# Optimization experiments

Measured on AMD Instinct MI355X. Metric: run time of the kernel, lower is better.

The kernel has to match this reference:

```python
import jax, jax.numpy as jnp
import numpy as np

NEG_SLOPE = 0.2  # PyG GATConv default negative_slope
EPS = 1e-16      # PyG softmax denominator eps


def gat_layer(x, src, dst, W, a_src, a_dst, num_nodes):
    """One GATConv (eval mode, self-loops already appended to src/dst).
    x: [N, Fin], W: [Fin, H*C], a_src/a_dst: [H, C]. Returns [N, H, C]."""
    H, C = a_src.shape
    h = (x @ W).reshape(num_nodes, H, C)                  # [N,H,C]
    alpha_src = jnp.sum(h * a_src, axis=-1)               # [N,H]
    alpha_dst = jnp.sum(h * a_dst, axis=-1)               # [N,H]
    e = alpha_src[src] + alpha_dst[dst]                   # [E,H]
    e = jnp.where(e > 0, e, NEG_SLOPE * e)                # leaky_relu
    # segment softmax keyed by destination node
    m = jax.ops.segment_max(e, dst, num_segments=num_nodes)   # [N,H]
    ex = jnp.exp(e - m[dst])                              # [E,H]
    s = jax.ops.segment_sum(ex, dst, num_segments=num_nodes)  # [N,H]
    alpha = ex / (s[dst] + EPS)                           # [E,H]
    # weighted scatter-aggregation of source features
    msg = h[src] * alpha[..., None]                       # [E,H,C]
    out = jax.ops.segment_sum(msg, dst, num_segments=num_nodes)  # [N,H,C]
    return out


def setup_inputs() -> dict:
    key = jax.random.key(0)
    ks = jax.random.split(key, 10)
    N, E = 50000, 800000
    Fin, C1, H, Fout = 128, 32, 8, 1
    x = jax.random.normal(ks[0], (N, Fin), dtype=jnp.float32)
    edge_index = jax.random.randint(ks[1], (2, E), 0, N).astype(jnp.int64)
    sc = 0.1
    W1 = jax.random.normal(ks[2], (Fin, H * C1), dtype=jnp.float32) * sc
    att_src1 = jax.random.normal(ks[3], (H, C1), dtype=jnp.float32) * sc
    att_dst1 = jax.random.normal(ks[4], (H, C1), dtype=jnp.float32) * sc
    bias1 = jnp.zeros((H * C1,), dtype=jnp.float32)
    W2 = jax.random.normal(ks[5], (H * C1, Fout), dtype=jnp.float32) * sc
    att_src2 = jax.random.normal(ks[6], (1, Fout), dtype=jnp.float32) * sc
    att_dst2 = jax.random.normal(ks[7], (1, Fout), dtype=jnp.float32) * sc
    bias2 = jnp.zeros((Fout,), dtype=jnp.float32)
    return {"x": x, "edge_index": edge_index, "W1": W1, "att_src1": att_src1,
            "att_dst1": att_dst1, "bias1": bias1, "W2": W2, "att_src2": att_src2,
            "att_dst2": att_dst2, "bias2": bias2}


def reference(x, edge_index, W1, att_src1, att_dst1, bias1, W2, att_src2, att_dst2, bias2):
    N = x.shape[0]
    loops = jnp.arange(N, dtype=edge_index.dtype)
    src = jnp.concatenate([edge_index[0], loops])   # add_self_loops=True
    dst = jnp.concatenate([edge_index[1], loops])
    # layer 1: heads=8, concat=True
    h1 = gat_layer(x, src, dst, W1, att_src1, att_dst1, N)      # [N,H,C1]
    h1 = h1.reshape(N, -1) + bias1                               # [N,H*C1]
    h1 = jax.nn.elu(h1)
    # layer 2: heads=1, concat=False (single head -> identity mean)
    h2 = gat_layer(h1, src, dst, W2, att_src2, att_dst2, N)      # [N,1,1]
    h2 = h2.reshape(N, -1) + bias2                               # [N,1]
    return jax.nn.sigmoid(h2).squeeze(-1)                        # [N]
```

## Files before the change

### kernel.cpp

```cpp
#include <hip/hip_runtime.h>
#include <math.h>

#define NEG_SLOPE 0.2f
#define GAT_EPS 1e-16f
#define NEG_BIG -3.0e38f
#define LOG2E 1.4426950408889634f
#define MAXDEG 96
#define BCAP 6144
#define CHUNK 2048
#define PREPB 136

typedef __attribute__((ext_vector_type(8))) short short8;
typedef __attribute__((ext_vector_type(4))) float floatx4;
typedef __attribute__((ext_vector_type(2))) float floatx2;

__device__ __forceinline__ float leaky(float v) {
    return v > 0.f ? v : NEG_SLOPE * v;
}
__device__ __forceinline__ unsigned short f2bf(float f) {
    unsigned u = __float_as_uint(f);
    unsigned r = u + 0x7FFFu + ((u >> 16) & 1u);
    return (unsigned short)(r >> 16);
}
__device__ __forceinline__ unsigned char f2fp8(float f) {
    return (unsigned char)(__builtin_amdgcn_cvt_pk_fp8_f32(f, f, 0, false) & 0xff);
}

__global__ __launch_bounds__(256) void prep_scatterA(
    const float* __restrict__ W1, const float* __restrict__ a_src,
    const float* __restrict__ a_dst, unsigned short* __restrict__ w1t,
    const int* __restrict__ ei, unsigned int* __restrict__ bucket_buf,
    int* __restrict__ bucket_cnt, int E, int ET)
{
    __shared__ int lhist[256];
    __shared__ int lbase[256];
    const int t = threadIdx.x;

    if (blockIdx.x < PREPB) {
        int idx = blockIdx.x * 256 + t;
        if (idx < 128 * 256) {
            int n = idx >> 7, k = idx & 127;
            w1t[idx] = f2bf(W1[(size_t)k * 256 + n]);
        }
        if (idx < 2048) {
            int j = idx >> 7, k = idx & 127;
            const float* a = (j < 8) ? (a_src + j * 32) : (a_dst + (j - 8) * 32);
            const float* wr = W1 + (size_t)k * 256 + (j & 7) * 32;
            float s = 0.f;
            #pragma unroll
            for (int c = 0; c < 32; ++c) s += wr[c] * a[c];
            w1t[(size_t)(256 + j) * 128 + k] = f2bf(s);
        }
        return;
    }

    lhist[t] = 0;
    __syncthreads();
    const int base = (blockIdx.x - PREPB) * CHUNK;
    unsigned int pk[8]; int bk[8], rk[8]; bool v[8];
    #pragma unroll
    for (int k = 0; k < 8; ++k) {
        int i = base + k * 256 + t;
        v[k] = i < ET;
        int ii = v[k] ? i : 0;
        int src = (ii < E) ? ei[ii] : (ii - E);
        int dst = (ii < E) ? ei[E + ii] : (ii - E);
        bk[k] = dst >> 8;
        pk[k] = ((unsigned)src << 8) | (unsigned)(dst & 255);
    }
    #pragma unroll
    for (int k = 0; k < 8; ++k)
        if (v[k]) rk[k] = atomicAdd(&lhist[bk[k]], 1);
    __syncthreads();
    if (lhist[t] > 0) lbase[t] = atomicAdd(&bucket_cnt[t], lhist[t]);
    __syncthreads();
    #pragma unroll
    for (int k = 0; k < 8; ++k) {
        if (v[k]) {
            int pos = lbase[bk[k]] + rk[k];
            if (pos < BCAP) bucket_buf[(size_t)bk[k] * BCAP + pos] = pk[k];
        }
    }
}

__global__ __launch_bounds__(256) void gemm_scatterB(
    const float* __restrict__ x, const unsigned short* __restrict__ w1t,
    unsigned char* __restrict__ h1b, float* __restrict__ as1, float* __restrict__ ad1,
    const unsigned int* __restrict__ bucket_buf, const int* __restrict__ bucket_cnt,
    int* __restrict__ cnt, unsigned short* __restrict__ csr_pad,
    int N, int ntiles)
{
    __shared__ __align__(16) unsigned short Asl[64][40];
    __shared__ __align__(16) unsigned short Bsl[272][40];
    __shared__ int lcnt[256];
    const int t = threadIdx.x;

    if (blockIdx.x >= ntiles) {
        const int b = blockIdx.x - ntiles;
        lcnt[t] = 0;
        __syncthreads();
        int tot = bucket_cnt[b]; if (tot > BCAP) tot = BCAP;
        const unsigned int* bp = bucket_buf + (size_t)b * BCAP;
        for (int j = t; j < tot; j += 256) {
            unsigned int e = bp[j];
            int loc = e & 255;
            int src = (int)(e >> 8);
            int slot = atomicAdd(&lcnt[loc], 1);
            if (slot < MAXDEG)
                csr_pad[(((size_t)b << 8) | loc) * MAXDEG + slot] = (unsigned short)src;
        }
        __syncthreads();
        int node = (b << 8) | t;
        if (node < N) cnt[node] = lcnt[t];
        return;
    }

    const int row0 = blockIdx.x * 64;
    const int wave = t >> 6, lane = t & 63;
    const int l15 = lane & 15, quad = lane >> 4;

    floatx4 acc[17];
    #pragma unroll
    for (int i = 0; i < 17; ++i) acc[i] = (floatx4){0.f, 0.f, 0.f, 0.f};

    for (int kc = 0; kc < 128; kc += 32) {
        {
            int r = t >> 2, q = t & 3;
            int row = row0 + r; if (row > N - 1) row = N - 1;
            const float4* xp = (const float4*)(x + (size_t)row * 128 + kc + q * 8);
            float4 f0 = xp[0], f1 = xp[1];
            ushort4 u0, u1;
            u0.x = f2bf(f0.x); u0.y = f2bf(f0.y); u0.z = f2bf(f0.z); u0.w = f2bf(f0.w);
            u1.x = f2bf(f1.x); u1.y = f2bf(f1.y); u1.z = f2bf(f1.z); u1.w = f2bf(f1.w);
            *(ushort4*)&Asl[r][q * 8] = u0;
            *(ushort4*)&Asl[r][q * 8 + 4] = u1;
        }
        {
            #pragma unroll
            for (int q = 0; q < 4; ++q) {
                uint4 v = *(const uint4*)&w1t[(size_t)t * 128 + kc + q * 8];
                *(uint4*)&Bsl[t][q * 8] = v;
            }
            if (t < 16) {
                #pragma unroll
                for (int q = 0; q < 4; ++q) {
                    uint4 v = *(const uint4*)&w1t[(size_t)(256 + t) * 128 + kc + q * 8];
                    *(uint4*)&Bsl[256 + t][q * 8] = v;
                }
            }
        }
        __syncthreads();
        short8 a = *(const short8*)&Asl[wave * 16 + l15][quad * 8];
        #pragma unroll
        for (int nt = 0; nt < 17; ++nt) {
            short8 bb = *(const short8*)&Bsl[nt * 16 + l15][quad * 8];
            acc[nt] = __builtin_amdgcn_mfma_f32_16x16x32_bf16(a, bb, acc[nt], 0, 0, 0);
        }
        __syncthreads();
    }
    #pragma unroll
    for (int reg = 0; reg < 4; ++reg) {
        int row = row0 + wave * 16 + quad * 4 + reg;
        if (row < N) {
            unsigned char* rp = h1b + ((size_t)row << 8);
            #pragma unroll
            for (int nt = 0; nt < 16; ++nt)
                rp[nt * 16 + l15] = f2fp8(acc[nt][reg]);
            float vv = acc[16][reg] * LOG2E;
            if (l15 < 8) as1[(size_t)row * 8 + l15] = vv;
            else         ad1[(size_t)row * 8 + l15 - 8] = vv;
        }
    }
}

__global__ __launch_bounds__(256) void aggr1_fused(
    const int* __restrict__ cnt, const unsigned short* __restrict__ csr_pad,
    const float* __restrict__ as1, const float* __restrict__ ad1,
    const unsigned char* __restrict__ h1b,
    const float* __restrict__ bias1, const float* __restrict__ W2,
    float* __restrict__ h2, int N)
{
    int n = blockIdx.x * 4 + (threadIdx.x >> 6);
    int lane = threadIdx.x & 63;
    if (n >= N) return;
    const size_t rs = (size_t)n * MAXDEG;
    int deg = cnt[n]; if (deg > MAXDEG) deg = MAXDEG;
    int le = lane >> 3, lh = lane & 7, hh = lane >> 3;
    float adv = ad1[(size_t)n * 8 + lh];

    int c0 = 0, c1 = 0;
    if (lane < deg)      c0 = csr_pad[rs + lane];
    if (64 + lane < deg) c1 = csr_pad[rs + 64 + lane];

    float m = NEG_BIG, s = 0.f;
    float4 acc = make_float4(0.f, 0.f, 0.f, 0.f);

    for (int j0 = 0; j0 < deg; j0 += 8) {
        int cc = (j0 < 64) ? c0 : c1;
        int bo = j0 & 63;
        int srcs[8];
        #pragma unroll
        for (int j = 0; j < 8; ++j) srcs[j] = __shfl(cc, bo + j);
        unsigned int hv[8];
        #pragma unroll
        for (int j = 0; j < 8; ++j)
            hv[j] = *(const unsigned int*)&h1b[((size_t)srcs[j] << 8) + lane * 4];
        float av = as1[(size_t)srcs[le] * 8 + lh];
        float l = (j0 + le < deg) ? leaky(av + adv) : NEG_BIG;
        float Mc = fmaxf(l, __shfl_xor(l, 8));
        Mc = fmaxf(Mc, __shfl_xor(Mc, 16));
        Mc = fmaxf(Mc, __shfl_xor(Mc, 32));
        if (__any(Mc > m + 8.f)) {
            float mn = fmaxf(m, Mc);
            float sc = exp2f(m - mn);
            s *= sc;
            float sca = __shfl(sc, hh);
            acc.x *= sca; acc.y *= sca; acc.z *= sca; acc.w *= sca;
            m = mn;
        }
        float p = exp2f(l - m);
        float ps = p + __shfl_xor(p, 8);
        ps += __shfl_xor(ps, 16);
        ps += __shfl_xor(ps, 32);
        s += ps;
        #pragma unroll
        for (int j = 0; j < 8; ++j) {
            float pj = __shfl(p, (j << 3) | hh);
            floatx2 lo = __builtin_amdgcn_cvt_pk_f32_fp8((int)hv[j], false);
            floatx2 hi = __builtin_amdgcn_cvt_pk_f32_fp8((int)hv[j], true);
            acc.x += pj * lo.x;
            acc.y += pj * lo.y;
            acc.z += pj * hi.x;
            acc.w += pj * hi.y;
        }
    }

    float sH = __shfl(s, hh);
    float inv = 1.f / (sH + GAT_EPS);
    acc.x *= inv; acc.y *= inv; acc.z *= inv; acc.w *= inv;

    float4 b = *(const float4*)&bias1[lane * 4];
    acc.x += b.x; acc.y += b.y; acc.z += b.z; acc.w += b.w;
    acc.x = acc.x > 0.f ? acc.x : __expf(acc.x) - 1.f;
    acc.y = acc.y > 0.f ? acc.y : __expf(acc.y) - 1.f;
    acc.z = acc.z > 0.f ? acc.z : __expf(acc.z) - 1.f;
    acc.w = acc.w > 0.f ? acc.w : __expf(acc.w) - 1.f;
    float4 w = *(const float4*)&W2[lane * 4];
    float part = acc.x * w.x + acc.y * w.y + acc.z * w.z + acc.w * w.w;
    #pragma unroll
    for (int mask = 1; mask < 64; mask <<= 1) part += __shfl_xor(part, mask);
    if (lane == 0) h2[n] = part;
}

__global__ __launch_bounds__(256) void layer2_fused(
    const int* __restrict__ cnt, const unsigned short* __restrict__ csr_pad,
    const float* __restrict__ h2, const float* __restrict__ a_s2,
    const float* __restrict__ a_d2, const float* __restrict__ bias2,
    float* __restrict__ out, int N)
{
    int n = blockIdx.x * 16 + (threadIdx.x >> 4);
    int sl = threadIdx.x & 15;
    if (n >= N) return;
    const size_t rs = (size_t)n * MAXDEG;
    int deg = cnt[n]; if (deg > MAXDEG) deg = MAXDEG;
    float asc = a_s2[0], adc = a_d2[0];
    float hdc = h2[n] * adc;

    float m = NEG_BIG, s = 0.f, acc = 0.f;
    for (int k = sl; k < deg; k += 16) {
        float hs = h2[csr_pad[rs + k]];
        float l = leaky(hs * asc + hdc);
        if (l > m) {
            float sc = __expf(m - l);
            s = s * sc + 1.f;
            acc = acc * sc + hs;
            m = l;
        } else {
            float p = __expf(l - m);
            s += p;
            acc += p * hs;
        }
    }
    #pragma unroll
    for (int mask = 1; mask < 16; mask <<= 1) {
        float mo = __shfl_xor(m, mask);
        float so = __shfl_xor(s, mask);
        float ao = __shfl_xor(acc, mask);
        float M = fmaxf(m, mo);
        float e1 = __expf(m - M), e2 = __expf(mo - M);
        s = s * e1 + so * e2;
        acc = acc * e1 + ao * e2;
        m = M;
    }
    if (sl == 0) {
        float z = acc / (s + GAT_EPS) + bias2[0];
        out[n] = 1.f / (1.f + __expf(-z));
    }
}

extern "C" void kernel_launch(void* const* d_in, const int* in_sizes, int n_in,
                              void* d_out, int out_size, void* d_ws, size_t ws_size,
                              hipStream_t stream)
{
    const float* x      = (const float*)d_in[0];
    const int*   ei     = (const int*)  d_in[1];
    const float* W1     = (const float*)d_in[2];
    const float* a_src1 = (const float*)d_in[3];
    const float* a_dst1 = (const float*)d_in[4];
    const float* bias1  = (const float*)d_in[5];
    const float* W2     = (const float*)d_in[6];
    const float* a_s2   = (const float*)d_in[7];
    const float* a_d2   = (const float*)d_in[8];
    const float* bias2  = (const float*)d_in[9];
    float* out = (float*)d_out;

    const int N  = in_sizes[0] / 128;
    const int E  = in_sizes[1] / 2;
    const int ET = E + N;
    const int ntiles   = (N + 63) / 64;
    const int nbuckets = (N + 255) >> 8;
    const int ablocks  = (ET + CHUNK - 1) / CHUNK;

    char* wsb = (char*)d_ws;
    size_t off = 0;
    auto walloc = [&](size_t bytes) -> void* {
        void* p = wsb + off;
        off += (bytes + 255) & ~(size_t)255;
        return p;
    };
    unsigned short* w1t     = (unsigned short*)walloc((size_t)272 * 128 * 2);
    unsigned char*  h1b     = (unsigned char*) walloc((size_t)N * 256);
    float*          as1     = (float*)         walloc((size_t)N * 8 * 4);
    float*          ad1     = (float*)         walloc((size_t)N * 8 * 4);
    float*          h2      = (float*)         walloc((size_t)N * 4);
    int*            cnt     = (int*)           walloc((size_t)N * 4);
    unsigned short* csr_pad = (unsigned short*)walloc((size_t)N * MAXDEG * 2);
    int*            bucket_cnt = (int*)        walloc(256 * 4);
    unsigned int*   bucket_buf = (unsigned int*)walloc((size_t)nbuckets * BCAP * 4);

    hipMemsetAsync(bucket_cnt, 0, 256 * sizeof(int), stream);

    prep_scatterA<<<PREPB + ablocks, 256, 0, stream>>>(W1, a_src1, a_dst1, w1t,
                                                       ei, bucket_buf, bucket_cnt, E, ET);

    gemm_scatterB<<<ntiles + nbuckets, 256, 0, stream>>>(x, w1t, h1b, as1, ad1,
                                                         bucket_buf, bucket_cnt,
                                                         cnt, csr_pad, N, ntiles);

    aggr1_fused<<<(N + 3) / 4, 256, 0, stream>>>(cnt, csr_pad, as1, ad1, h1b,
                                                 bias1, W2, h2, N);
    layer2_fused<<<(N + 15) / 16, 256, 0, stream>>>(cnt, csr_pad, h2,
                                                    a_s2, a_d2, bias2, out, N);
}
```

Baseline: 178.9 us.

## Prefetch attention logits upfront and double-buffer feature gathers in aggr1

The layer-1 aggregation kernel now loads every per-edge source attention score into a register array before the loop, and fully unrolls the tile loop with ping-pong register buffers. Each iteration issues the next tile's fp8 feature gathers before processing the current tile. The aim is to hide the latency of the irregular global gathers behind the online-softmax and accumulate math. The cost is higher register pressure (12 attention values plus two 8-word buffers), which may lower occupancy, and a larger fully unrolled body.

```diff
diff --git a/kernel.cpp b/kernel.cpp
--- a/kernel.cpp
+++ b/kernel.cpp
@@ -6,6 +6,7 @@
 #define NEG_BIG -3.0e38f
 #define LOG2E 1.4426950408889634f
 #define MAXDEG 96
+#define MAXTILE 12
 #define BCAP 6144
 #define CHUNK 2048
 #define PREPB 136
@@ -173,6 +174,47 @@
     }
 }
 
+#define AGATHER(T, HV) {                                                            \
+    int j0g = (T) * 8;                                                              \
+    int ccg = (j0g < 64) ? c0 : c1;                                                 \
+    int bog = j0g & 63;                                                             \
+    _Pragma("unroll")                                                               \
+    for (int j = 0; j < 8; ++j) {                                                   \
+        int sj = __shfl(ccg, bog + j);                                              \
+        HV[j] = *(const unsigned int*)&h1b[((size_t)sj << 8) + lane * 4];           \
+    }                                                                               \
+}
+
+#define APROC(T, HV) {                                                              \
+    float l = ((T) * 8 + le < deg) ? leaky(avv[(T)] + adv) : NEG_BIG;               \
+    float Mc = fmaxf(l, __shfl_xor(l, 8));                                          \
+    Mc = fmaxf(Mc, __shfl_xor(Mc, 16));                                             \
+    Mc = fmaxf(Mc, __shfl_xor(Mc, 32));                                             \
+    if (__any(Mc > m + 8.f)) {                                                      \
+        float mn = fmaxf(m, Mc);                                                    \
+        float sc = exp2f(m - mn);                                                   \
+        s *= sc;                                                                    \
+        float sca = __shfl(sc, hh);                                                 \
+        acc.x *= sca; acc.y *= sca; acc.z *= sca; acc.w *= sca;                     \
+        m = mn;                                                                     \
+    }                                                                               \
+    float p = exp2f(l - m);                                                         \
+    float ps = p + __shfl_xor(p, 8);                                                \
+    ps += __shfl_xor(ps, 16);                                                       \
+    ps += __shfl_xor(ps, 32);                                                       \
+    s += ps;                                                                        \
+    _Pragma("unroll")                                                               \
+    for (int j = 0; j < 8; ++j) {                                                   \
+        float pj = __shfl(p, (j << 3) | hh);                                        \
+        floatx2 lo = __builtin_amdgcn_cvt_pk_f32_fp8((int)HV[j], false);            \
+        floatx2 hi = __builtin_amdgcn_cvt_pk_f32_fp8((int)HV[j], true);             \
+        acc.x += pj * lo.x;                                                         \
+        acc.y += pj * lo.y;                                                         \
+        acc.z += pj * hi.x;                                                         \
+        acc.w += pj * hi.y;                                                         \
+    }                                                                               \
+}
+
 __global__ __launch_bounds__(256) void aggr1_fused(
     const int* __restrict__ cnt, const unsigned short* __restrict__ csr_pad,
     const float* __restrict__ as1, const float* __restrict__ ad1,
@@ -192,46 +234,35 @@
     if (lane < deg)      c0 = csr_pad[rs + lane];
     if (64 + lane < deg) c1 = csr_pad[rs + 64 + lane];
 
+    const int ntile = (deg + 7) >> 3;
+
+    float avv[MAXTILE];
+    #pragma unroll
+    for (int t = 0; t < MAXTILE; ++t) {
+        avv[t] = 0.f;
+        if (t < ntile) {
+            int j0g = t * 8;
+            int ccg = (j0g < 64) ? c0 : c1;
+            int sle = __shfl(ccg, (j0g & 63) + le);
+            avv[t] = as1[(size_t)sle * 8 + lh];
+        }
+    }
+
     float m = NEG_BIG, s = 0.f;
     float4 acc = make_float4(0.f, 0.f, 0.f, 0.f);
 
-    for (int j0 = 0; j0 < deg; j0 += 8) {
-        int cc = (j0 < 64) ? c0 : c1;
-        int bo = j0 & 63;
-        int srcs[8];
-        #pragma unroll
-        for (int j = 0; j < 8; ++j) srcs[j] = __shfl(cc, bo + j);
-        unsigned int hv[8];
-        #pragma unroll
-        for (int j = 0; j < 8; ++j)
-            hv[j] = *(const unsigned int*)&h1b[((size_t)srcs[j] << 8) + lane * 4];
-        float av = as1[(size_t)srcs[le] * 8 + lh];
-        float l = (j0 + le < deg) ? leaky(av + adv) : NEG_BIG;
-        float Mc = fmaxf(l, __shfl_xor(l, 8));
-        Mc = fmaxf(Mc, __shfl_xor(Mc, 16));
-        Mc = fmaxf(Mc, __shfl_xor(Mc, 32));
-        if (__any(Mc > m + 8.f)) {
-            float mn = fmaxf(m, Mc);
-            float sc = exp2f(m - mn);
-            s *= sc;
-            float sca = __shfl(sc, hh);
-            acc.x *= sca; acc.y *= sca; acc.z *= sca; acc.w *= sca;
-            m = mn;
-        }
-        float p = exp2f(l - m);
-        float ps = p + __shfl_xor(p, 8);
-        ps += __shfl_xor(ps, 16);
-        ps += __shfl_xor(ps, 32);
-        s += ps;
-        #pragma unroll
-        for (int j = 0; j < 8; ++j) {
-            float pj = __shfl(p, (j << 3) | hh);
-            floatx2 lo = __builtin_amdgcn_cvt_pk_f32_fp8((int)hv[j], false);
-            floatx2 hi = __builtin_amdgcn_cvt_pk_f32_fp8((int)hv[j], true);
-            acc.x += pj * lo.x;
-            acc.y += pj * lo.y;
-            acc.z += pj * hi.x;
-            acc.w += pj * hi.y;
+    unsigned int hvA[8], hvB[8];
+    AGATHER(0, hvA);
+    #pragma unroll
+    for (int tp = 0; tp < MAXTILE / 2; ++tp) {
+        const int t0 = tp * 2, t1 = tp * 2 + 1;
+        if (t0 < ntile) {
+            if (t1 < ntile) AGATHER(t1, hvB);
+            APROC(t0, hvA);
+        }
+        if (t1 < ntile) {
+            if (t1 + 1 < ntile) AGATHER(t1 + 1, hvA);
+            APROC(t1, hvB);
         }
     }
 
```

New measurement: 191.1 us. 1.07x slower.
